# Kernel tuning notes

Hardware: AMD Instinct MI355X
Metric: run time of the kernel (lower is better)

## Reference

```python
import jax, jax.numpy as jnp
import numpy as np
from jax import lax

LN_EPS = 1e-5
DENOM_EPS = 1e-6


def taylor_exp(x, f):
    # x: [..., f] -> [..., 1 + f + f*f]
    r2 = np.sqrt(2.0).astype(np.float32)
    rd = np.sqrt(float(f)).astype(np.float32)
    rrd = np.sqrt(np.sqrt(float(f))).astype(np.float32)
    x2 = (x[..., :, None] * x[..., None, :]).reshape(*x.shape[:-1], f * f) / r2
    return jnp.concatenate([jnp.ones_like(x[..., :1]), x / rrd, x2 / rd], axis=-1)


def layer_norm(x, gamma, beta):
    mu = jnp.mean(x, axis=-1, keepdims=True)
    var = jnp.mean(jnp.square(x - mu), axis=-1, keepdims=True)
    return (x - mu) * lax.rsqrt(var + LN_EPS) * gamma + beta


def setup_inputs() -> dict:
    key = jax.random.key(0)
    ks = jax.random.split(key, 24)
    B, L, d, h, f, hd, w = 4, 2048, 1024, 16, 16, 64, 64
    D = 1 + f + f * f  # 273

    def lin_w(k, fi, fo):
        return (jax.random.normal(k, (fi, fo), jnp.float32) / np.sqrt(fi)).astype(jnp.float32)

    def lin_b(k, fo):
        return 0.01 * jax.random.normal(k, (fo,), jnp.float32)

    inp = {
        'x': jax.random.normal(ks[0], (B, L, d), jnp.float32),
        'kv_state': jnp.zeros((B, h, D, hd), jnp.float32),
        'k_state': jnp.zeros((B, h, D), jnp.float32),
        'k_buf': jnp.zeros((1, h, w, hd), jnp.float32),
        'v_buf': jnp.zeros((1, h, w, hd), jnp.float32),
        # LinearAttention projections
        'Wq_lin': lin_w(ks[1], d, f * h), 'bq_lin': lin_b(ks[2], f * h),
        'Wk_lin': lin_w(ks[3], d, f * h), 'bk_lin': lin_b(ks[4], f * h),
        'Wv_lin': lin_w(ks[5], d, hd * h), 'bv_lin': lin_b(ks[6], hd * h),
        'Wo_lin': lin_w(ks[7], d, d), 'bo_lin': lin_b(ks[8], d),
        # BasedBlock window-attention projections
        'Wq': lin_w(ks[9], d, d), 'bq': lin_b(ks[10], d),
        'Wk': lin_w(ks[11], d, d), 'bk': lin_b(ks[12], d),
        'Wv': lin_w(ks[13], d, d), 'bv': lin_b(ks[14], d),
        'Wo': lin_w(ks[15], d, d), 'bo': lin_b(ks[16], d),
        # shared LayerNorm
        'gamma': jnp.ones((d,), jnp.float32),
        'beta': jnp.zeros((d,), jnp.float32),
    }
    return inp


def reference(x, kv_state, k_state, k_buf, v_buf,
              Wq_lin, bq_lin, Wk_lin, bk_lin, Wv_lin, bv_lin, Wo_lin, bo_lin,
              Wq, bq, Wk, bk, Wv, bv, Wo, bo, gamma, beta):
    B, L, d = x.shape
    h = kv_state.shape[1]
    hd = kv_state.shape[3]
    f = Wq_lin.shape[1] // h

    # ---- LinearAttention ----
    q = (x @ Wq_lin + bq_lin).reshape(B, L, h, f).transpose(0, 2, 1, 3)   # b h l f
    k = (x @ Wk_lin + bk_lin).reshape(B, L, h, f).transpose(0, 2, 1, 3)
    v = (x @ Wv_lin + bv_lin).reshape(B, L, h, hd).transpose(0, 2, 1, 3)  # b h l hd
    qf = taylor_exp(q, f)  # b h l D
    kf = taylor_exp(k, f)

    # time-major for scan: [l, b, h, ...]
    qt = qf.transpose(2, 0, 1, 3)
    kt = kf.transpose(2, 0, 1, 3)
    vt = v.transpose(2, 0, 1, 3)

    def step(carry, inp):
        kv, kst = carry
        q_t, k_t, v_t = inp
        kv = kv + k_t[..., :, None] * v_t[..., None, :]            # b h D hd
        kst = kst + k_t                                            # b h D
        num = jnp.einsum('bhd,bhdc->bhc', q_t, kv)
        den = jnp.einsum('bhd,bhd->bh', q_t, kst) + DENOM_EPS
        return (kv, kst), num / den[..., None]

    (kv_new, k_new), outs = lax.scan(step, (kv_state, k_state), (qt, kt, vt))
    lin = outs.transpose(1, 0, 2, 3).reshape(B, L, h * hd)  # b l (h hd)
    lin_out = lin @ Wo_lin + bo_lin  # dropout is identity in eval

    x1 = layer_norm(x + lin_out, gamma, beta)

    # ---- window attention ----
    q2 = (x1 @ Wq + bq).reshape(B, L, h, hd).transpose(0, 2, 1, 3)  # b h l hd
    k2 = (x1 @ Wk + bk).reshape(B, L, h, hd).transpose(0, 2, 1, 3)
    v2 = (x1 @ Wv + bv).reshape(B, L, h, hd).transpose(0, 2, 1, 3)

    new_k = k2[:, :, -1:, :]
    new_v = v2[:, :, -1:, :]
    kb = jnp.broadcast_to(k_buf, (B,) + k_buf.shape[1:])
    vb = jnp.broadcast_to(v_buf, (B,) + v_buf.shape[1:])
    uk = jnp.concatenate([kb[:, :, 1:], new_k], axis=2)  # b h w hd
    uv = jnp.concatenate([vb[:, :, 1:], new_v], axis=2)

    scores = jnp.einsum('bhqd,bhwd->bhqw', q2, uk) / np.sqrt(float(hd))
    attn = jax.nn.softmax(scores, axis=-1)
    win = jnp.einsum('bhqw,bhwd->bhqd', attn, uv)
    win = win.transpose(0, 2, 1, 3).reshape(B, L, h * hd)

    out = layer_norm(x1 + (win @ Wo + bo), gamma, beta)
    return out, kv_new, k_new
```

## Files before the change

### kernel.cpp

```cpp
#include <hip/hip_runtime.h>
#include <math.h>


#define LL 2048
#define DD 1024
#define DFEAT 273
#define NC 16
#define CHUNK 128

typedef __attribute__((ext_vector_type(8))) short short8;
typedef __attribute__((ext_vector_type(4))) float f32x4;

#define SQ 0.42044820762685725f
#define LF 1.18920711500272107f

__device__ __forceinline__ float4 f4(float a, float b, float c, float d) {
  float4 r; r.x = a; r.y = b; r.z = c; r.w = d; return r;
}

__device__ __forceinline__ unsigned short f2bf(float f) {
  union { float f; unsigned u; } v; v.f = f;
  unsigned r = v.u + 0x7fffu + ((v.u >> 16) & 1u);
  return (unsigned short)(r >> 16);
}

__device__ __forceinline__ float bf2f(unsigned short u) {
  union { unsigned u; float f; } v; v.u = ((unsigned)u) << 16; return v.f;
}

__global__ __launch_bounds__(256) void cast_bf16(
    const float* __restrict__ in, unsigned short* __restrict__ o, int n4) {
  int i = blockIdx.x * 256 + threadIdx.x;
  if (i < n4) {
    float4 v = ((const float4*)in)[i];
    ushort4 r;
    r.x = f2bf(v.x); r.y = f2bf(v.y); r.z = f2bf(v.z); r.w = f2bf(v.w);
    ((ushort4*)o)[i] = r;
  }
}

__global__ __launch_bounds__(256) void castT(
    const float* __restrict__ W, unsigned short* __restrict__ Wt, int K, int N) {
  __shared__ float t[64][65];
  int k0 = blockIdx.x * 64, n0 = blockIdx.y * 64;
  int tid = threadIdx.x;
#pragma unroll
  for (int p = 0; p < 16; p++) {
    int idx = p * 256 + tid;
    int r = idx >> 6, c = idx & 63;
    t[r][c] = W[(size_t)(k0 + r) * N + n0 + c];
  }
  __syncthreads();
#pragma unroll
  for (int p = 0; p < 16; p++) {
    int idx = p * 256 + tid;
    int rn = idx >> 6, ck = idx & 63;
    Wt[(size_t)(n0 + rn) * K + k0 + ck] = f2bf(t[ck][rn]);
  }
}

__global__ __launch_bounds__(256) void gemm_mfma(
    const unsigned short* __restrict__ A, const unsigned short* __restrict__ Bt,
    const float* __restrict__ bias, float* __restrict__ C,
    unsigned short* __restrict__ Cb, int M, int N, int K) {
  __shared__ unsigned short As[128 * 64];
  __shared__ unsigned short Bs[128 * 64];
  const int tid = threadIdx.x;
  const int lane = tid & 63, w = tid >> 6;
  const int row0 = blockIdx.x * 128, col0 = blockIdx.y * 128;
  const int wm0 = (w & 1) * 64, wn0 = (w >> 1) * 64;
  const int lr = lane >> 3;
  const int gc = (lane & 7) ^ lr;
  const unsigned short* aP = A + (size_t)(row0 + w * 32 + lr) * K + gc * 8;
  const unsigned short* bP = Bt + (size_t)(col0 + w * 32 + lr) * K + gc * 8;
  unsigned short* asW = As + w * 2048;
  unsigned short* bsW = Bs + w * 2048;
  const int m15 = lane & 15, quad = lane >> 4;
  f32x4 acc[4][4] = {};
  for (int k0 = 0; k0 < K; k0 += 64) {
#pragma unroll
    for (int i = 0; i < 4; i++) {
      __builtin_amdgcn_global_load_lds(
          (const __attribute__((address_space(1))) unsigned int*)(const void*)(aP + (size_t)(i * 8) * K + k0),
          (__attribute__((address_space(3))) unsigned int*)(void*)(asW + i * 512), 16, 0, 0);
      __builtin_amdgcn_global_load_lds(
          (const __attribute__((address_space(1))) unsigned int*)(const void*)(bP + (size_t)(i * 8) * K + k0),
          (__attribute__((address_space(3))) unsigned int*)(void*)(bsW + i * 512), 16, 0, 0);
    }
    __syncthreads();
#pragma unroll
    for (int ks = 0; ks < 2; ks++) {
      short8 aF[4], bF[4];
#pragma unroll
      for (int mi = 0; mi < 4; mi++) {
        int r = wm0 + mi * 16 + m15;
        int g = (ks * 4 + quad) ^ (r & 7);
        aF[mi] = *(const short8*)(As + r * 64 + g * 8);
      }
#pragma unroll
      for (int ni = 0; ni < 4; ni++) {
        int r = wn0 + ni * 16 + m15;
        int g = (ks * 4 + quad) ^ (r & 7);
        bF[ni] = *(const short8*)(Bs + r * 64 + g * 8);
      }
#pragma unroll
      for (int mi = 0; mi < 4; mi++)
#pragma unroll
        for (int ni = 0; ni < 4; ni++)
          acc[mi][ni] = __builtin_amdgcn_mfma_f32_16x16x32_bf16(
              aF[mi], bF[ni], acc[mi][ni], 0, 0, 0);
    }
    __syncthreads();
  }
#pragma unroll
  for (int mi = 0; mi < 4; mi++)
#pragma unroll
    for (int ni = 0; ni < 4; ni++) {
      int col = col0 + wn0 + ni * 16 + m15;
      float bb = bias[col];
#pragma unroll
      for (int r = 0; r < 4; r++) {
        int row = row0 + wm0 + mi * 16 + quad * 4 + r;
        float val = acc[mi][ni][r] + bb;
        if (Cb) Cb[(size_t)row * N + col] = f2bf(val);
        else C[(size_t)row * N + col] = val;
      }
    }
}

__global__ __launch_bounds__(256) void transV(
    const unsigned short* __restrict__ v_b, unsigned short* __restrict__ vT) {
  __shared__ unsigned short Tv[64][72];
  const int blk = blockIdx.x;
  const int bh = blk >> 5, tt = blk & 31;
  const int b = bh >> 4, hh = bh & 15;
  const int t0 = tt * 64;
  const int tid = threadIdx.x;
  {
    int t = tid >> 2, cs = tid & 3;
    const unsigned short* p = v_b + ((size_t)(b * LL + t0 + t)) * DD + hh * 64 + cs * 16;
    *(short8*)&Tv[t][cs * 16] = *(const short8*)p;
    *(short8*)&Tv[t][cs * 16 + 8] = *(const short8*)(p + 8);
  }
  __syncthreads();
  {
    int c = tid & 63, ts = tid >> 6;
    unsigned short vals[16];
#pragma unroll
    for (int j = 0; j < 16; j++) vals[j] = Tv[ts * 16 + j][c];
    unsigned short* op = vT + ((size_t)bh * 64 + c) * LL + t0 + ts * 16;
    *(short8*)op = *(short8*)&vals[0];
    *(short8*)(op + 8) = *(short8*)&vals[8];
  }
}

__global__ __launch_bounds__(256) void phaseA2(
    const unsigned short* __restrict__ klin, const unsigned short* __restrict__ vT,
    unsigned short* __restrict__ KVc_t, unsigned short* __restrict__ kstc) {
  __shared__ unsigned short kT[16][136];
  const int tid = threadIdx.x, lane = tid & 63, w = tid >> 6;
  const int m15 = lane & 15, quad = lane >> 4;
  const int bh = blockIdx.x >> 4, ck = blockIdx.x & 15;
  const int b = bh >> 4, hh = bh & 15;
  const int t0 = ck * CHUNK;
  {
    int r = tid >> 1, half = tid & 1;
    short8 kv = *(const short8*)(klin + ((size_t)(b * LL + t0 + r)) * 256 + hh * 16 + half * 8);
#pragma unroll
    for (int j = 0; j < 8; j++)
      kT[half * 8 + j][r] = f2bf(bf2f(((unsigned short*)&kv)[j]) * SQ);
  }
  __syncthreads();
  short8 ones8 = {16256, 16256, 16256, 16256, 16256, 16256, 16256, 16256};
  short8 zer8 = {0, 0, 0, 0, 0, 0, 0, 0};
  f32x4 acc[5][5] = {};
  const unsigned short* vbase = vT + (size_t)bh * 64 * LL + t0;
#pragma unroll
  for (int ks = 0; ks < 4; ++ks) {
    const int tt = ks * 32 + quad * 8;
    short8 aF[5], bF[5];
#pragma unroll
    for (int mi = 0; mi < 5; mi++) {
      int r = (w * 5 + mi) * 16 + m15;
      short8 av;
      unsigned short* pv = (unsigned short*)&av;
      if (r == 0) {
        av = ones8;
      } else if (r < 17) {
        short8 k1 = *(const short8*)&kT[r - 1][tt];
#pragma unroll
        for (int j = 0; j < 8; j++) pv[j] = f2bf(bf2f(((unsigned short*)&k1)[j]) * LF);
      } else if (r < DFEAT) {
        int ij = r - 17;
        short8 k1 = *(const short8*)&kT[ij >> 4][tt];
        short8 k2 = *(const short8*)&kT[ij & 15][tt];
#pragma unroll
        for (int j = 0; j < 8; j++)
          pv[j] = f2bf(bf2f(((unsigned short*)&k1)[j]) * bf2f(((unsigned short*)&k2)[j]));
      } else {
        av = zer8;
      }
      aF[mi] = av;
    }
#pragma unroll
    for (int ni = 0; ni < 4; ni++)
      bF[ni] = *(const short8*)(vbase + ((size_t)(ni * 16 + m15)) * LL + tt);
    bF[4] = (m15 == 0) ? ones8 : zer8;
#pragma unroll
    for (int mi = 0; mi < 5; mi++)
#pragma unroll
      for (int ni = 0; ni < 5; ni++)
        acc[mi][ni] = __builtin_amdgcn_mfma_f32_16x16x32_bf16(
            aF[mi], bF[ni], acc[mi][ni], 0, 0, 0);
  }
  const size_t cb = ((size_t)bh * NC + ck) * (64 * 288);
  const size_t kb = ((size_t)bh * NC + ck) * 288;
#pragma unroll
  for (int mi = 0; mi < 5; mi++) {
    int fb = (w * 5 + mi) * 16 + quad * 4;
    if (fb < 288) {
#pragma unroll
      for (int ni = 0; ni < 4; ni++) {
        int c = ni * 16 + m15;
        ushort4 sv;
        sv.x = f2bf(acc[mi][ni][0]); sv.y = f2bf(acc[mi][ni][1]);
        sv.z = f2bf(acc[mi][ni][2]); sv.w = f2bf(acc[mi][ni][3]);
        *(ushort4*)(KVc_t + cb + (size_t)c * 288 + fb) = sv;
      }
      if (m15 == 0) {
        ushort4 sv;
        sv.x = f2bf(acc[mi][4][0]); sv.y = f2bf(acc[mi][4][1]);
        sv.z = f2bf(acc[mi][4][2]); sv.w = f2bf(acc[mi][4][3]);
        *(ushort4*)(kstc + kb + fb) = sv;
      }
    }
  }
}

__global__ __launch_bounds__(256) void phaseB3(
    const unsigned short* __restrict__ KVc_t, const unsigned short* __restrict__ kstc,
    const float* __restrict__ kv0, const float* __restrict__ kst0,
    unsigned short* __restrict__ KVp_t, unsigned short* __restrict__ kstp,
    float* __restrict__ kv_out, float* __restrict__ kst_out) {
  const int tid = threadIdx.x;
  if (blockIdx.x < 576) {
    int gid = blockIdx.x * 256 + tid;
    int bh = gid / 2304, rem = gid - bh * 2304;
    int c = rem / 36, fg = rem - c * 36;
    int f0 = fg * 8;
    float acc[8];
#pragma unroll
    for (int j = 0; j < 8; j++) {
      int f = f0 + j;
      acc[j] = (f < DFEAT) ? kv0[((size_t)bh * DFEAT + f) * 64 + c] : 0.0f;
    }
    size_t base = ((size_t)bh * NC) * (64 * 288) + (size_t)c * 288 + f0;
    for (int ck = 0; ck < NC; ck++) {
      size_t idx = base + (size_t)ck * (64 * 288);
      short8 t = *(const short8*)(KVc_t + idx);
      unsigned short ov[8];
#pragma unroll
      for (int j = 0; j < 8; j++) {
        ov[j] = f2bf(acc[j]);
        acc[j] += bf2f(((unsigned short*)&t)[j]);
      }
      *(short8*)(KVp_t + idx) = *(short8*)ov;
    }
#pragma unroll
    for (int j = 0; j < 8; j++) {
      int f = f0 + j;
      if (f < DFEAT) kv_out[((size_t)bh * DFEAT + f) * 64 + c] = acc[j];
    }
  } else {
    int idx0 = (blockIdx.x - 576) * 256 + tid;
    int bh = idx0 / 36, fg = idx0 - bh * 36;
    int f0 = fg * 8;
    float acc[8];
#pragma unroll
    for (int j = 0; j < 8; j++) {
      int f = f0 + j;
      acc[j] = (f < DFEAT) ? kst0[bh * DFEAT + f] : 0.0f;
    }
    for (int ck = 0; ck < NC; ck++) {
      size_t idx = ((size_t)bh * NC + ck) * 288 + f0;
      short8 t = *(const short8*)(kstc + idx);
      unsigned short ov[8];
#pragma unroll
      for (int j = 0; j < 8; j++) {
        ov[j] = f2bf(acc[j]);
        acc[j] += bf2f(((unsigned short*)&t)[j]);
      }
      *(short8*)(kstp + idx) = *(short8*)ov;
    }
#pragma unroll
    for (int j = 0; j < 8; j++) {
      int f = f0 + j;
      if (f < DFEAT) kst_out[bh * DFEAT + f] = acc[j];
    }
  }
}

__global__ __launch_bounds__(256) void phaseC4(
    const unsigned short* __restrict__ qlin, const unsigned short* __restrict__ klin,
    const unsigned short* __restrict__ vT, const unsigned short* __restrict__ KVp_t,
    const unsigned short* __restrict__ kstp, unsigned short* __restrict__ outs) {
  __shared__ float qs[4][32][36];
  __shared__ unsigned short S_l[4][32 * 128];
  const int tid = threadIdx.x, lane = tid & 63, w = tid >> 6;
  const int m15 = lane & 15, quad = lane >> 4;
  const int bh = blockIdx.x >> 4, ck = blockIdx.x & 15;
  const int qw = w;
  const int b = bh >> 4, hh = bh & 15;
  const int t0 = ck * CHUNK;
  const int tr0 = qw * 32;
  float (*qsw)[36] = qs[w];
  unsigned short* Sw = S_l[w];
  const unsigned short* qbase = qlin + ((size_t)(b * LL + t0 + tr0)) * 256 + hh * 16;
  const unsigned short* kbase = klin + ((size_t)(b * LL + t0)) * 256 + hh * 16;
  {
    int r = lane >> 1, h8 = lane & 1;
    short8 qv = *(const short8*)(qbase + (size_t)r * 256 + h8 * 8);
    float qf[8];
#pragma unroll
    for (int j = 0; j < 8; j++) qf[j] = bf2f(((unsigned short*)&qv)[j]) * SQ;
    *(float4*)&qsw[r][h8 * 8] = f4(qf[0], qf[1], qf[2], qf[3]);
    *(float4*)&qsw[r][h8 * 8 + 4] = f4(qf[4], qf[5], qf[6], qf[7]);
#pragma unroll
    for (int j = 0; j < 8; j++)
      qsw[r][16 + ((h8 * 8 + j + 9) & 15)] = qf[j];
  }
  short8 ones8 = {16256, 16256, 16256, 16256, 16256, 16256, 16256, 16256};
  short8 zer8 = {0, 0, 0, 0, 0, 0, 0, 0};
  f32x4 acc[2][5] = {};
  const unsigned short* KVb = KVp_t + ((size_t)(bh * NC + ck)) * (64 * 288);
  const unsigned short* kstb = kstp + ((size_t)(bh * NC + ck)) * 288;
#pragma unroll
  for (int ks = 0; ks < 9; ++ks) {
    const int fs = ks * 32 + quad * 8;
    short8 aF[2], bF[5];
#pragma unroll
    for (int ni = 0; ni < 4; ni++)
      bF[ni] = *(const short8*)(KVb + ((size_t)(ni * 16 + m15)) * 288 + fs);
    bF[4] = (m15 == 0) ? *(const short8*)(kstb + fs) : zer8;
#pragma unroll
    for (int mi = 0; mi < 2; mi++) {
      const float* qr = &qsw[mi * 16 + m15][0];
      unsigned short pv[8];
      if (ks == 0) {
        float qr0 = qr[0];
#pragma unroll
        for (int j = 0; j < 8; j++) {
          int f = (quad << 3) + j;
          int fl = f - 1; fl = fl < 0 ? 0 : fl;
          int fm = f - 17; fm = fm < 0 ? 0 : fm;
          float lin = qr[fl] * LF;
          float prod = qr0 * qr[fm];
          float val = (f == 0) ? 1.0f : ((f < 17) ? lin : prod);
          pv[j] = f2bf(val);
        }
      } else {
        int base = fs - 17;
        int i0 = base >> 4;
        float qi0 = qr[i0];
        float qi1 = qr[i0 + 1];
        const float* qv = qr + 16 + (base & 8);
        float qj[8];
        *(float4*)&qj[0] = *(const float4*)qv;
        *(float4*)&qj[4] = *(const float4*)(qv + 4);
        float qiB = (quad & 1) ? qi0 : qi1;
#pragma unroll
        for (int j = 0; j < 8; j++) {
          float qi = (j == 0) ? qi0 : qiB;
          float val = qi * qj[j];
          if (ks == 8) val = ((quad << 3) + j < 17) ? val : 0.0f;
          pv[j] = f2bf(val);
        }
      }
      aF[mi] = *(short8*)pv;
    }
#pragma unroll
    for (int mi = 0; mi < 2; mi++)
#pragma unroll
      for (int ni = 0; ni < 5; ni++)
        acc[mi][ni] = __builtin_amdgcn_mfma_f32_16x16x32_bf16(
            aF[mi], bF[ni], acc[mi][ni], 0, 0, 0);
  }
  const int nsn = 2 * qw + 2;
  {
    short8 aU[2], bU[8];
    aU[0] = (quad < 2) ? *(const short8*)(qbase + (size_t)m15 * 256 + quad * 8) : zer8;
    aU[1] = (quad < 2) ? *(const short8*)(qbase + (size_t)(16 + m15) * 256 + quad * 8) : zer8;
#pragma unroll
    for (int sn = 0; sn < 8; sn++) {
      if (sn < nsn) {
        int s = sn * 16 + m15;
        bU[sn] = (quad < 2) ? *(const short8*)(kbase + (size_t)s * 256 + quad * 8) : zer8;
      }
    }
#pragma unroll
    for (int mi = 0; mi < 2; mi++) {
#pragma unroll
      for (int sn = 0; sn < 8; sn++) {
        if (sn < nsn) {
          f32x4 zz = {0.f, 0.f, 0.f, 0.f};
          f32x4 u = __builtin_amdgcn_mfma_f32_16x16x32_bf16(aU[mi], bU[sn], zz, 0, 0, 0);
          int s = sn * 16 + m15;
          int gRow = s >> 3;
#pragma unroll
          for (int rr = 0; rr < 4; rr++) {
            int tl = mi * 16 + quad * 4 + rr;
            int tc = tr0 + tl;
            float uu = u[rr];
            float sv = (s <= tc) ? fmaf(uu, fmaf(uu, 0.03125f, 0.25f), 1.0f) : 0.0f;
            int p = gRow ^ (tl & 7);
            Sw[tl * 128 + p * 8 + (s & 7)] = f2bf(sv);
          }
        }
      }
    }
  }
  const unsigned short* vbase = vT + (size_t)bh * 64 * LL + t0;
#pragma unroll
  for (int ks = 0; ks < 4; ++ks) {
    if (ks <= qw) {
      const int tt = ks * 32 + quad * 8;
      short8 aF[2], bF[5];
#pragma unroll
      for (int mi = 0; mi < 2; mi++) {
        int tl = mi * 16 + m15;
        int p = (ks * 4 + quad) ^ (tl & 7);
        aF[mi] = *(const short8*)&Sw[tl * 128 + p * 8];
      }
#pragma unroll
      for (int ni = 0; ni < 4; ni++)
        bF[ni] = *(const short8*)(vbase + ((size_t)(ni * 16 + m15)) * LL + tt);
      bF[4] = (m15 == 0) ? ones8 : zer8;
#pragma unroll
      for (int mi = 0; mi < 2; mi++)
#pragma unroll
        for (int ni = 0; ni < 5; ni++)
          acc[mi][ni] = __builtin_amdgcn_mfma_f32_16x16x32_bf16(
              aF[mi], bF[ni], acc[mi][ni], 0, 0, 0);
    }
  }
#pragma unroll
  for (int mi = 0; mi < 2; mi++) {
#pragma unroll
    for (int rr = 0; rr < 4; rr++) {
      float den = __shfl(acc[mi][4][rr], (lane & 48));
      float inv = 1.0f / (den + 1e-6f);
      int tl = mi * 16 + quad * 4 + rr;
      unsigned short* op = outs + ((size_t)(b * LL + t0 + tr0 + tl)) * DD + hh * 64;
#pragma unroll
      for (int ni = 0; ni < 4; ni++)
        op[ni * 16 + m15] = f2bf(acc[mi][ni][rr] * inv);
    }
  }
}

__global__ __launch_bounds__(256) void lastrow_init(
    const float* __restrict__ bk, const float* __restrict__ bv,
    float* __restrict__ klast, float* __restrict__ vlast) {
  int gid = blockIdx.x * 256 + threadIdx.x;
  int which = gid >> 12;
  int b = (gid >> 10) & 3;
  int n = gid & 1023;
  (which ? vlast : klast)[b * 1024 + n] = which ? bv[n] : bk[n];
}

__global__ __launch_bounds__(256) void lastrow_qkv2(
    const float* __restrict__ x1,
    const float* __restrict__ Wk, const float* __restrict__ Wv,
    float* __restrict__ klast, float* __restrict__ vlast) {
  __shared__ float xs[4][64];
  __shared__ float red[4][4][64];
  const int blk = blockIdx.x;
  const int which = blk >> 8;
  const int nstrip = (blk >> 4) & 15;
  const int kslice = blk & 15;
  const int n0 = nstrip * 64, k0 = kslice * 64;
  const int tid = threadIdx.x;
  const int nn = tid & 63, p = tid >> 6;
  {
    int b = tid >> 6, k = tid & 63;
    xs[b][k] = x1[((size_t)(b * LL + LL - 1)) * DD + k0 + k];
  }
  __syncthreads();
  const float* W = which ? Wv : Wk;
  float acc[4] = {};
#pragma unroll
  for (int i = 0; i < 16; i++) {
    int kk = p * 16 + i;
    float wv = W[(size_t)(k0 + kk) * 1024 + n0 + nn];
#pragma unroll
    for (int b = 0; b < 4; b++) acc[b] = fmaf(xs[b][kk], wv, acc[b]);
  }
#pragma unroll
  for (int b = 0; b < 4; b++) red[p][b][nn] = acc[b];
  __syncthreads();
  if (p == 0) {
    float* outp = which ? vlast : klast;
#pragma unroll
    for (int b = 0; b < 4; b++) {
      float s = red[0][b][nn] + red[1][b][nn] + red[2][b][nn] + red[3][b][nn];
      atomicAdd(outp + b * 1024 + n0 + nn, s);
    }
  }
}

__global__ __launch_bounds__(256) void prep_window(
    const float* __restrict__ kbuf, const float* __restrict__ vbufw,
    const float* __restrict__ klast, const float* __restrict__ vlast,
    unsigned short* __restrict__ ukb, unsigned short* __restrict__ uvT) {
  __shared__ float Tv[64][68];
  const int bh = blockIdx.x;
  const int b = bh >> 4, hh = bh & 15;
  const int tid = threadIdx.x;
  const int wi = tid >> 2, d0 = (tid & 3) * 16;
  {
    const float* kp = (wi < 63) ? (kbuf + ((size_t)hh * 64 + wi + 1) * 64 + d0)
                                : (klast + (size_t)b * 1024 + hh * 64 + d0);
    unsigned short* op = ukb + ((size_t)bh * 64 + wi) * 64 + d0;
#pragma unroll
    for (int j4 = 0; j4 < 4; j4++) {
      float4 v = *(const float4*)(kp + j4 * 4);
      ushort4 r;
      r.x = f2bf(v.x); r.y = f2bf(v.y); r.z = f2bf(v.z); r.w = f2bf(v.w);
      *(ushort4*)(op + j4 * 4) = r;
    }
  }
  {
    const float* vp = (wi < 63) ? (vbufw + ((size_t)hh * 64 + wi + 1) * 64 + d0)
                                : (vlast + (size_t)b * 1024 + hh * 64 + d0);
#pragma unroll
    for (int j4 = 0; j4 < 4; j4++)
      *(float4*)&Tv[wi][d0 + j4 * 4] = *(const float4*)(vp + j4 * 4);
  }
  __syncthreads();
  {
    int c = tid & 63, w0 = (tid >> 6) * 16;
    unsigned short* op = uvT + ((size_t)bh * 64 + c) * 64 + w0;
    unsigned short vals[16];
#pragma unroll
    for (int j = 0; j < 16; j++) vals[j] = f2bf(Tv[w0 + j][c]);
    *(short8*)op = *(short8*)&vals[0];
    *(short8*)(op + 8) = *(short8*)&vals[8];
  }
}

__global__ __launch_bounds__(256) void window_attn2(
    const unsigned short* __restrict__ q2b, const unsigned short* __restrict__ ukb,
    const unsigned short* __restrict__ uvT, unsigned short* __restrict__ win) {
  __shared__ unsigned short S_l[128 * 64];
  const int tid = threadIdx.x, lane = tid & 63, w = tid >> 6;
  const int m15 = lane & 15, quad = lane >> 4;
  const int bh = blockIdx.x >> 4, tile = blockIdx.x & 15;
  const int b = bh >> 4, hh = bh & 15;
  const int t0 = tile * 128 + w * 32;
  const unsigned short* ukbase = ukb + (size_t)bh * 64 * 64;
  const unsigned short* uvbase = uvT + (size_t)bh * 64 * 64;
  f32x4 accS[2][4] = {};
#pragma unroll
  for (int ks = 0; ks < 2; ks++) {
    short8 aF[2], bF[4];
#pragma unroll
    for (int mi = 0; mi < 2; mi++)
      aF[mi] = *(const short8*)(q2b + ((size_t)(b * LL + t0 + mi * 16 + m15)) * DD +
                                hh * 64 + ks * 32 + quad * 8);
#pragma unroll
    for (int ni = 0; ni < 4; ni++)
      bF[ni] = *(const short8*)(ukbase + ((size_t)(ni * 16 + m15)) * 64 + ks * 32 + quad * 8);
#pragma unroll
    for (int mi = 0; mi < 2; mi++)
#pragma unroll
      for (int ni = 0; ni < 4; ni++)
        accS[mi][ni] = __builtin_amdgcn_mfma_f32_16x16x32_bf16(
            aF[mi], bF[ni], accS[mi][ni], 0, 0, 0);
  }
#pragma unroll
  for (int mi = 0; mi < 2; mi++) {
#pragma unroll
    for (int rr = 0; rr < 4; rr++) {
      float s0 = accS[mi][0][rr] * 0.125f;
      float s1 = accS[mi][1][rr] * 0.125f;
      float s2 = accS[mi][2][rr] * 0.125f;
      float s3 = accS[mi][3][rr] * 0.125f;
      float m = fmaxf(fmaxf(s0, s1), fmaxf(s2, s3));
      m = fmaxf(m, __shfl_xor(m, 1));
      m = fmaxf(m, __shfl_xor(m, 2));
      m = fmaxf(m, __shfl_xor(m, 4));
      m = fmaxf(m, __shfl_xor(m, 8));
      float p0 = __expf(s0 - m), p1 = __expf(s1 - m);
      float p2 = __expf(s2 - m), p3 = __expf(s3 - m);
      float l = p0 + p1 + p2 + p3;
      l += __shfl_xor(l, 1);
      l += __shfl_xor(l, 2);
      l += __shfl_xor(l, 4);
      l += __shfl_xor(l, 8);
      float inv = 1.0f / l;
      int tl = w * 32 + mi * 16 + quad * 4 + rr;
      int t7 = tl & 7;
      float pr[4] = {p0 * inv, p1 * inv, p2 * inv, p3 * inv};
#pragma unroll
      for (int ni = 0; ni < 4; ni++) {
        int s = ni * 16 + m15;
        S_l[tl * 64 + ((s >> 3) ^ t7) * 8 + (s & 7)] = f2bf(pr[ni]);
      }
    }
  }
  f32x4 accO[2][4] = {};
#pragma unroll
  for (int ks = 0; ks < 2; ks++) {
    short8 aF[2], bF[4];
#pragma unroll
    for (int mi = 0; mi < 2; mi++) {
      int tl = w * 32 + mi * 16 + m15;
      int g = (ks * 4 + quad) ^ (tl & 7);
      aF[mi] = *(const short8*)&S_l[tl * 64 + g * 8];
    }
#pragma unroll
    for (int ni = 0; ni < 4; ni++)
      bF[ni] = *(const short8*)(uvbase + ((size_t)(ni * 16 + m15)) * 64 + ks * 32 + quad * 8);
#pragma unroll
    for (int mi = 0; mi < 2; mi++)
#pragma unroll
      for (int ni = 0; ni < 4; ni++)
        accO[mi][ni] = __builtin_amdgcn_mfma_f32_16x16x32_bf16(
            aF[mi], bF[ni], accO[mi][ni], 0, 0, 0);
  }
#pragma unroll
  for (int mi = 0; mi < 2; mi++) {
#pragma unroll
    for (int rr = 0; rr < 4; rr++) {
      int row = t0 + mi * 16 + quad * 4 + rr;
      unsigned short* op = win + ((size_t)(b * LL + row)) * DD + hh * 64;
#pragma unroll
      for (int ni = 0; ni < 4; ni++)
        op[ni * 16 + m15] = f2bf(accO[mi][ni][rr]);
    }
  }
}

__global__ __launch_bounds__(256) void ln_add(
    const float* __restrict__ A, const float* __restrict__ Bm,
    const float* __restrict__ gamma, const float* __restrict__ beta,
    float* __restrict__ out, unsigned short* __restrict__ outb) {
  const int row = blockIdx.x, tid = threadIdx.x;
  float4 va = ((const float4*)(A + (size_t)row * DD))[tid];
  float4 vb = ((const float4*)(Bm + (size_t)row * DD))[tid];
  float4 s4 = f4(va.x + vb.x, va.y + vb.y, va.z + vb.z, va.w + vb.w);
  float s = s4.x + s4.y + s4.z + s4.w;
  float ss = s4.x * s4.x + s4.y * s4.y + s4.z * s4.z + s4.w * s4.w;
  for (int o = 32; o; o >>= 1) { s += __shfl_xor(s, o); ss += __shfl_xor(ss, o); }
  __shared__ float red[8];
  int wid = tid >> 6;
  if ((tid & 63) == 0) { red[wid * 2] = s; red[wid * 2 + 1] = ss; }
  __syncthreads();
  float tot = red[0] + red[2] + red[4] + red[6];
  float tots = red[1] + red[3] + red[5] + red[7];
  float mu = tot * (1.0f / 1024.0f);
  float var = tots * (1.0f / 1024.0f) - mu * mu;
  float rstd = rsqrtf(var + 1e-5f);
  float4 g = ((const float4*)gamma)[tid];
  float4 be = ((const float4*)beta)[tid];
  float4 o = f4((s4.x - mu) * rstd * g.x + be.x, (s4.y - mu) * rstd * g.y + be.y,
                (s4.z - mu) * rstd * g.z + be.z, (s4.w - mu) * rstd * g.w + be.w);
  ((float4*)(out + (size_t)row * DD))[tid] = o;
  if (outb) {
    ushort4 r;
    r.x = f2bf(o.x); r.y = f2bf(o.y); r.z = f2bf(o.z); r.w = f2bf(o.w);
    ((ushort4*)(outb + (size_t)row * DD))[tid] = r;
  }
}

extern "C" void kernel_launch(void* const* d_in, const int* in_sizes, int n_in,
                              void* d_out, int out_size, void* d_ws, size_t ws_size,
                              hipStream_t stream) {
  (void)in_sizes; (void)n_in; (void)out_size; (void)ws_size;
  const float* x      = (const float*)d_in[0];
  const float* kv0    = (const float*)d_in[1];
  const float* kst0   = (const float*)d_in[2];
  const float* kbuf   = (const float*)d_in[3];
  const float* vbufw  = (const float*)d_in[4];
  const float* Wq_lin = (const float*)d_in[5];
  const float* bq_lin = (const float*)d_in[6];
  const float* Wk_lin = (const float*)d_in[7];
  const float* bk_lin = (const float*)d_in[8];
  const float* Wv_lin = (const float*)d_in[9];
  const float* bv_lin = (const float*)d_in[10];
  const float* Wo_lin = (const float*)d_in[11];
  const float* bo_lin = (const float*)d_in[12];
  const float* Wq     = (const float*)d_in[13];
  const float* bq     = (const float*)d_in[14];
  const float* Wk     = (const float*)d_in[15];
  const float* bk     = (const float*)d_in[16];
  const float* Wv     = (const float*)d_in[17];
  const float* bv     = (const float*)d_in[18];
  const float* Wo     = (const float*)d_in[19];
  const float* bo     = (const float*)d_in[20];
  const float* gamma  = (const float*)d_in[21];
  const float* beta   = (const float*)d_in[22];

  float* out = (float*)d_out;
  float* kv_out  = out + 8388608;
  float* kst_out = out + 8388608 + 1118208;

  float* ws = (float*)d_ws;
  const size_t MF = 1024 * 1024;
  unsigned short* qlin_b = (unsigned short*)(ws);
  unsigned short* klin_b = (unsigned short*)(ws + 1 * MF);
  unsigned short* v_b    = (unsigned short*)(ws + 2 * MF);
  unsigned short* vT     = (unsigned short*)(ws + 6 * MF);
  unsigned short* KVc_t  = (unsigned short*)(ws + 10 * MF);
  unsigned short* kstc   = (unsigned short*)(ws + 19 * MF);
  unsigned short* KVp_t  = (unsigned short*)(ws + 20 * MF);
  unsigned short* kstp   = (unsigned short*)(ws + 29 * MF);
  unsigned short* x_bf   = (unsigned short*)(ws + 30 * MF);
  unsigned short* outs_bf = (unsigned short*)(ws + 2 * MF);
  float* tmp  = ws + 10 * MF;
  float* x1   = ws + 20 * MF;
  unsigned short* x1b = (unsigned short*)(ws + 30 * MF);
  unsigned short* q2b = (unsigned short*)ws;
  unsigned short* winb = (unsigned short*)(ws + 8 * MF);
  float* tmp2 = ws + 12 * MF;
  float* klast = ws + 34 * MF;
  float* vlast = klast + 4096;
  unsigned short* ukb = (unsigned short*)(ws + 34 * MF + 8192);
  unsigned short* uvTw = ukb + 262144;
  unsigned short* WtQL = (unsigned short*)(ws + 35 * MF);
  unsigned short* WtKL = WtQL + 262144;
  unsigned short* WtVL = WtQL + 524288;
  unsigned short* WtO1 = WtQL + 1572864;
  unsigned short* WtQ2 = WtQL + 2621440;
  unsigned short* WtO2 = WtQL + 3670016;

  dim3 blk(256);
  cast_bf16<<<8192, blk, 0, stream>>>(x, x_bf, 2097152);
  castT<<<dim3(16, 4), blk, 0, stream>>>(Wq_lin, WtQL, 1024, 256);
  castT<<<dim3(16, 4), blk, 0, stream>>>(Wk_lin, WtKL, 1024, 256);
  castT<<<dim3(16, 16), blk, 0, stream>>>(Wv_lin, WtVL, 1024, 1024);
  castT<<<dim3(16, 16), blk, 0, stream>>>(Wo_lin, WtO1, 1024, 1024);
  castT<<<dim3(16, 16), blk, 0, stream>>>(Wq, WtQ2, 1024, 1024);
  castT<<<dim3(16, 16), blk, 0, stream>>>(Wo, WtO2, 1024, 1024);
  gemm_mfma<<<dim3(64, 2), blk, 0, stream>>>(x_bf, WtQL, bq_lin, (float*)0, qlin_b, 8192, 256, 1024);
  gemm_mfma<<<dim3(64, 2), blk, 0, stream>>>(x_bf, WtKL, bk_lin, (float*)0, klin_b, 8192, 256, 1024);
  gemm_mfma<<<dim3(64, 8), blk, 0, stream>>>(x_bf, WtVL, bv_lin, (float*)0, v_b, 8192, 1024, 1024);
  transV<<<2048, blk, 0, stream>>>(v_b, vT);
  phaseA2<<<1024, blk, 0, stream>>>(klin_b, vT, KVc_t, kstc);
  phaseB3<<<585, blk, 0, stream>>>(KVc_t, kstc, kv0, kst0, KVp_t, kstp, kv_out, kst_out);
  phaseC4<<<1024, blk, 0, stream>>>(qlin_b, klin_b, vT, KVp_t, kstp, outs_bf);
  gemm_mfma<<<dim3(64, 8), blk, 0, stream>>>(outs_bf, WtO1, bo_lin, tmp, (unsigned short*)0, 8192, 1024, 1024);
  ln_add<<<8192, blk, 0, stream>>>(x, tmp, gamma, beta, x1, x1b);
  gemm_mfma<<<dim3(64, 8), blk, 0, stream>>>(x1b, WtQ2, bq, (float*)0, q2b, 8192, 1024, 1024);
  lastrow_init<<<32, blk, 0, stream>>>(bk, bv, klast, vlast);
  lastrow_qkv2<<<512, blk, 0, stream>>>(x1, Wk, Wv, klast, vlast);
  prep_window<<<64, blk, 0, stream>>>(kbuf, vbufw, klast, vlast, ukb, uvTw);
  window_attn2<<<1024, blk, 0, stream>>>(q2b, ukb, uvTw, winb);
  gemm_mfma<<<dim3(64, 8), blk, 0, stream>>>(winb, WtO2, bo, tmp2, (unsigned short*)0, 8192, 1024, 1024);
  ln_add<<<8192, blk, 0, stream>>>(x1, tmp2, gamma, beta, out, (unsigned short*)0);
}
```

Measured before the change: 443.4 us.

## Fuse QKV projection GEMMs, batch weight casts, and use bf16 intermediates

Merges the six weight-transpose-cast launches into one kernel that also concatenates the q/k/v biases. The three linear-attention projections become a single N=1536 GEMM, and downstream kernels index into the combined output. The output-projection GEMMs and the first layernorm now write bf16 instead of fp32, and the second layernorm and last-row projection read the bf16 x1. This cuts launch count and memory traffic, at the cost of extra bf16 rounding in the residual path (x1 is now kept only in bf16).

```diff
diff --git a/kernel.cpp b/kernel.cpp
--- a/kernel.cpp
+++ b/kernel.cpp
@@ -7,6 +7,7 @@
 #define DFEAT 273
 #define NC 16
 #define CHUNK 128
+#define QKVN 1536
 
 typedef __attribute__((ext_vector_type(8))) short short8;
 typedef __attribute__((ext_vector_type(4))) float f32x4;
@@ -39,11 +40,31 @@
   }
 }
 
-__global__ __launch_bounds__(256) void castT(
-    const float* __restrict__ W, unsigned short* __restrict__ Wt, int K, int N) {
+__global__ __launch_bounds__(256) void castT_all(
+    const float* __restrict__ Wql, const float* __restrict__ Wkl,
+    const float* __restrict__ Wvl, const float* __restrict__ Wo1,
+    const float* __restrict__ Wq2, const float* __restrict__ Wo2,
+    const float* __restrict__ bql, const float* __restrict__ bkl,
+    const float* __restrict__ bvl,
+    unsigned short* __restrict__ Wcomb, unsigned short* __restrict__ WtO1,
+    unsigned short* __restrict__ WtQ2, unsigned short* __restrict__ WtO2,
+    float* __restrict__ bqkv) {
   __shared__ float t[64][65];
-  int k0 = blockIdx.x * 64, n0 = blockIdx.y * 64;
-  int tid = threadIdx.x;
+  const int blk = blockIdx.x, tid = threadIdx.x;
+  if (blk < 6) {
+    int i = blk * 256 + tid;
+    float v = (i < 256) ? bql[i] : (i < 512) ? bkl[i - 256] : bvl[i - 512];
+    bqkv[i] = v;
+  }
+  const float* W; unsigned short* Wt; int N, t0;
+  if (blk < 64)       { W = Wql; Wt = Wcomb;               N = 256;  t0 = blk; }
+  else if (blk < 128) { W = Wkl; Wt = Wcomb + 256 * 1024;  N = 256;  t0 = blk - 64; }
+  else if (blk < 384) { W = Wvl; Wt = Wcomb + 512 * 1024;  N = 1024; t0 = blk - 128; }
+  else if (blk < 640) { W = Wo1; Wt = WtO1;                N = 1024; t0 = blk - 384; }
+  else if (blk < 896) { W = Wq2; Wt = WtQ2;                N = 1024; t0 = blk - 640; }
+  else                { W = Wo2; Wt = WtO2;                N = 1024; t0 = blk - 896; }
+  const int nt = N >> 6;
+  const int k0 = (t0 / nt) * 64, n0 = (t0 % nt) * 64;
 #pragma unroll
   for (int p = 0; p < 16; p++) {
     int idx = p * 256 + tid;
@@ -55,7 +76,7 @@
   for (int p = 0; p < 16; p++) {
     int idx = p * 256 + tid;
     int rn = idx >> 6, ck = idx & 63;
-    Wt[(size_t)(n0 + rn) * K + k0 + ck] = f2bf(t[ck][rn]);
+    Wt[(size_t)(n0 + rn) * 1024 + k0 + ck] = f2bf(t[ck][rn]);
   }
 }
 
@@ -129,7 +150,7 @@
 }
 
 __global__ __launch_bounds__(256) void transV(
-    const unsigned short* __restrict__ v_b, unsigned short* __restrict__ vT) {
+    const unsigned short* __restrict__ qkv, unsigned short* __restrict__ vT) {
   __shared__ unsigned short Tv[64][72];
   const int blk = blockIdx.x;
   const int bh = blk >> 5, tt = blk & 31;
@@ -138,7 +159,7 @@
   const int tid = threadIdx.x;
   {
     int t = tid >> 2, cs = tid & 3;
-    const unsigned short* p = v_b + ((size_t)(b * LL + t0 + t)) * DD + hh * 64 + cs * 16;
+    const unsigned short* p = qkv + ((size_t)(b * LL + t0 + t)) * QKVN + 512 + hh * 64 + cs * 16;
     *(short8*)&Tv[t][cs * 16] = *(const short8*)p;
     *(short8*)&Tv[t][cs * 16 + 8] = *(const short8*)(p + 8);
   }
@@ -155,7 +176,7 @@
 }
 
 __global__ __launch_bounds__(256) void phaseA2(
-    const unsigned short* __restrict__ klin, const unsigned short* __restrict__ vT,
+    const unsigned short* __restrict__ qkv, const unsigned short* __restrict__ vT,
     unsigned short* __restrict__ KVc_t, unsigned short* __restrict__ kstc) {
   __shared__ unsigned short kT[16][136];
   const int tid = threadIdx.x, lane = tid & 63, w = tid >> 6;
@@ -165,7 +186,7 @@
   const int t0 = ck * CHUNK;
   {
     int r = tid >> 1, half = tid & 1;
-    short8 kv = *(const short8*)(klin + ((size_t)(b * LL + t0 + r)) * 256 + hh * 16 + half * 8);
+    short8 kv = *(const short8*)(qkv + ((size_t)(b * LL + t0 + r)) * QKVN + 256 + hh * 16 + half * 8);
 #pragma unroll
     for (int j = 0; j < 8; j++)
       kT[half * 8 + j][r] = f2bf(bf2f(((unsigned short*)&kv)[j]) * SQ);
@@ -301,7 +322,7 @@
 }
 
 __global__ __launch_bounds__(256) void phaseC4(
-    const unsigned short* __restrict__ qlin, const unsigned short* __restrict__ klin,
+    const unsigned short* __restrict__ qkv,
     const unsigned short* __restrict__ vT, const unsigned short* __restrict__ KVp_t,
     const unsigned short* __restrict__ kstp, unsigned short* __restrict__ outs) {
   __shared__ float qs[4][32][36];
@@ -315,11 +336,11 @@
   const int tr0 = qw * 32;
   float (*qsw)[36] = qs[w];
   unsigned short* Sw = S_l[w];
-  const unsigned short* qbase = qlin + ((size_t)(b * LL + t0 + tr0)) * 256 + hh * 16;
-  const unsigned short* kbase = klin + ((size_t)(b * LL + t0)) * 256 + hh * 16;
+  const unsigned short* qbase = qkv + ((size_t)(b * LL + t0 + tr0)) * QKVN + hh * 16;
+  const unsigned short* kbase = qkv + ((size_t)(b * LL + t0)) * QKVN + 256 + hh * 16;
   {
     int r = lane >> 1, h8 = lane & 1;
-    short8 qv = *(const short8*)(qbase + (size_t)r * 256 + h8 * 8);
+    short8 qv = *(const short8*)(qbase + (size_t)r * QKVN + h8 * 8);
     float qf[8];
 #pragma unroll
     for (int j = 0; j < 8; j++) qf[j] = bf2f(((unsigned short*)&qv)[j]) * SQ;
@@ -388,13 +409,13 @@
   const int nsn = 2 * qw + 2;
   {
     short8 aU[2], bU[8];
-    aU[0] = (quad < 2) ? *(const short8*)(qbase + (size_t)m15 * 256 + quad * 8) : zer8;
-    aU[1] = (quad < 2) ? *(const short8*)(qbase + (size_t)(16 + m15) * 256 + quad * 8) : zer8;
+    aU[0] = (quad < 2) ? *(const short8*)(qbase + (size_t)m15 * QKVN + quad * 8) : zer8;
+    aU[1] = (quad < 2) ? *(const short8*)(qbase + (size_t)(16 + m15) * QKVN + quad * 8) : zer8;
 #pragma unroll
     for (int sn = 0; sn < 8; sn++) {
       if (sn < nsn) {
         int s = sn * 16 + m15;
-        bU[sn] = (quad < 2) ? *(const short8*)(kbase + (size_t)s * 256 + quad * 8) : zer8;
+        bU[sn] = (quad < 2) ? *(const short8*)(kbase + (size_t)s * QKVN + quad * 8) : zer8;
       }
     }
 #pragma unroll
@@ -469,7 +490,7 @@
 }
 
 __global__ __launch_bounds__(256) void lastrow_qkv2(
-    const float* __restrict__ x1,
+    const unsigned short* __restrict__ x1b,
     const float* __restrict__ Wk, const float* __restrict__ Wv,
     float* __restrict__ klast, float* __restrict__ vlast) {
   __shared__ float xs[4][64];
@@ -483,7 +504,7 @@
   const int nn = tid & 63, p = tid >> 6;
   {
     int b = tid >> 6, k = tid & 63;
-    xs[b][k] = x1[((size_t)(b * LL + LL - 1)) * DD + k0 + k];
+    xs[b][k] = bf2f(x1b[((size_t)(b * LL + LL - 1)) * DD + k0 + k]);
   }
   __syncthreads();
   const float* W = which ? Wv : Wk;
@@ -641,14 +662,22 @@
   }
 }
 
-__global__ __launch_bounds__(256) void ln_add(
-    const float* __restrict__ A, const float* __restrict__ Bm,
+__global__ __launch_bounds__(256) void ln_add2(
+    const float* __restrict__ Af, const unsigned short* __restrict__ Ab,
+    const unsigned short* __restrict__ Bmb,
     const float* __restrict__ gamma, const float* __restrict__ beta,
     float* __restrict__ out, unsigned short* __restrict__ outb) {
   const int row = blockIdx.x, tid = threadIdx.x;
-  float4 va = ((const float4*)(A + (size_t)row * DD))[tid];
-  float4 vb = ((const float4*)(Bm + (size_t)row * DD))[tid];
-  float4 s4 = f4(va.x + vb.x, va.y + vb.y, va.z + vb.z, va.w + vb.w);
+  float a0, a1, a2, a3;
+  if (Af) {
+    float4 va = ((const float4*)(Af + (size_t)row * DD))[tid];
+    a0 = va.x; a1 = va.y; a2 = va.z; a3 = va.w;
+  } else {
+    ushort4 ua = ((const ushort4*)(Ab + (size_t)row * DD))[tid];
+    a0 = bf2f(ua.x); a1 = bf2f(ua.y); a2 = bf2f(ua.z); a3 = bf2f(ua.w);
+  }
+  ushort4 ub = ((const ushort4*)(Bmb + (size_t)row * DD))[tid];
+  float4 s4 = f4(a0 + bf2f(ub.x), a1 + bf2f(ub.y), a2 + bf2f(ub.z), a3 + bf2f(ub.w));
   float s = s4.x + s4.y + s4.z + s4.w;
   float ss = s4.x * s4.x + s4.y * s4.y + s4.z * s4.z + s4.w * s4.w;
   for (int o = 32; o; o >>= 1) { s += __shfl_xor(s, o); ss += __shfl_xor(ss, o); }
@@ -665,7 +694,7 @@
   float4 be = ((const float4*)beta)[tid];
   float4 o = f4((s4.x - mu) * rstd * g.x + be.x, (s4.y - mu) * rstd * g.y + be.y,
                 (s4.z - mu) * rstd * g.z + be.z, (s4.w - mu) * rstd * g.w + be.w);
-  ((float4*)(out + (size_t)row * DD))[tid] = o;
+  if (out) ((float4*)(out + (size_t)row * DD))[tid] = o;
   if (outb) {
     ushort4 r;
     r.x = f2bf(o.x); r.y = f2bf(o.y); r.z = f2bf(o.z); r.w = f2bf(o.w);
@@ -707,55 +736,46 @@
 
   float* ws = (float*)d_ws;
   const size_t MF = 1024 * 1024;
-  unsigned short* qlin_b = (unsigned short*)(ws);
-  unsigned short* klin_b = (unsigned short*)(ws + 1 * MF);
-  unsigned short* v_b    = (unsigned short*)(ws + 2 * MF);
-  unsigned short* vT     = (unsigned short*)(ws + 6 * MF);
-  unsigned short* KVc_t  = (unsigned short*)(ws + 10 * MF);
-  unsigned short* kstc   = (unsigned short*)(ws + 19 * MF);
-  unsigned short* KVp_t  = (unsigned short*)(ws + 20 * MF);
-  unsigned short* kstp   = (unsigned short*)(ws + 29 * MF);
-  unsigned short* x_bf   = (unsigned short*)(ws + 30 * MF);
-  unsigned short* outs_bf = (unsigned short*)(ws + 2 * MF);
-  float* tmp  = ws + 10 * MF;
-  float* x1   = ws + 20 * MF;
-  unsigned short* x1b = (unsigned short*)(ws + 30 * MF);
-  unsigned short* q2b = (unsigned short*)ws;
-  unsigned short* winb = (unsigned short*)(ws + 8 * MF);
-  float* tmp2 = ws + 12 * MF;
-  float* klast = ws + 34 * MF;
+  unsigned short* x_bf   = (unsigned short*)(ws);
+  unsigned short* qkv_b  = (unsigned short*)(ws + 4 * MF);
+  unsigned short* vT     = (unsigned short*)(ws + 10 * MF);
+  unsigned short* KVc_t  = (unsigned short*)(ws + 14 * MF);
+  unsigned short* kstc   = (unsigned short*)(ws + 23 * MF);
+  unsigned short* KVp_t  = (unsigned short*)(ws + 24 * MF);
+  unsigned short* kstp   = (unsigned short*)(ws + 33 * MF);
+  unsigned short* outs_bf = (unsigned short*)(ws + 34 * MF);
+  unsigned short* tmp_b  = (unsigned short*)(ws + 38 * MF);
+  unsigned short* x1b    = (unsigned short*)(ws + 42 * MF);
+  unsigned short* q2b    = (unsigned short*)(ws + 46 * MF);
+  unsigned short* winb   = (unsigned short*)(ws + 50 * MF);
+  unsigned short* tmp2_b = (unsigned short*)(ws + 54 * MF);
+  float* klast = ws + 58 * MF;
   float* vlast = klast + 4096;
-  unsigned short* ukb = (unsigned short*)(ws + 34 * MF + 8192);
+  unsigned short* ukb  = (unsigned short*)(ws + 58 * MF + 8192);
   unsigned short* uvTw = ukb + 262144;
-  unsigned short* WtQL = (unsigned short*)(ws + 35 * MF);
-  unsigned short* WtKL = WtQL + 262144;
-  unsigned short* WtVL = WtQL + 524288;
-  unsigned short* WtO1 = WtQL + 1572864;
-  unsigned short* WtQ2 = WtQL + 2621440;
-  unsigned short* WtO2 = WtQL + 3670016;
+  unsigned short* Wcomb = (unsigned short*)(ws + 59 * MF);
+  unsigned short* WtO1  = (unsigned short*)(ws + 60 * MF);
+  unsigned short* WtQ2  = (unsigned short*)(ws + 61 * MF);
+  unsigned short* WtO2  = (unsigned short*)(ws + 62 * MF);
+  float* bqkv = ws + 63 * MF;
 
   dim3 blk(256);
   cast_bf16<<<8192, blk, 0, stream>>>(x, x_bf, 2097152);
-  castT<<<dim3(16, 4), blk, 0, stream>>>(Wq_lin, WtQL, 1024, 256);
-  castT<<<dim3(16, 4), blk, 0, stream>>>(Wk_lin, WtKL, 1024, 256);
-  castT<<<dim3(16, 16), blk, 0, stream>>>(Wv_lin, WtVL, 1024, 1024);
-  castT<<<dim3(16, 16), blk, 0, stream>>>(Wo_lin, WtO1, 1024, 1024);
-  castT<<<dim3(16, 16), blk, 0, stream>>>(Wq, WtQ2, 1024, 1024);
-  castT<<<dim3(16, 16), blk, 0, stream>>>(Wo, WtO2, 1024, 1024);
-  gemm_mfma<<<dim3(64, 2), blk, 0, stream>>>(x_bf, WtQL, bq_lin, (float*)0, qlin_b, 8192, 256, 1024);
-  gemm_mfma<<<dim3(64, 2), blk, 0, stream>>>(x_bf, WtKL, bk_lin, (float*)0, klin_b, 8192, 256, 1024);
-  gemm_mfma<<<dim3(64, 8), blk, 0, stream>>>(x_bf, WtVL, bv_lin, (float*)0, v_b, 8192, 1024, 1024);
-  transV<<<2048, blk, 0, stream>>>(v_b, vT);
-  phaseA2<<<1024, blk, 0, stream>>>(klin_b, vT, KVc_t, kstc);
+  castT_all<<<1152, blk, 0, stream>>>(Wq_lin, Wk_lin, Wv_lin, Wo_lin, Wq, Wo,
+                                      bq_lin, bk_lin, bv_lin,
+                                      Wcomb, WtO1, WtQ2, WtO2, bqkv);
+  gemm_mfma<<<dim3(64, 12), blk, 0, stream>>>(x_bf, Wcomb, bqkv, (float*)0, qkv_b, 8192, QKVN, 1024);
+  transV<<<2048, blk, 0, stream>>>(qkv_b, vT);
+  phaseA2<<<1024, blk, 0, stream>>>(qkv_b, vT, KVc_t, kstc);
   phaseB3<<<585, blk, 0, stream>>>(KVc_t, kstc, kv0, kst0, KVp_t, kstp, kv_out, kst_out);
-  phaseC4<<<1024, blk, 0, stream>>>(qlin_b, klin_b, vT, KVp_t, kstp, outs_bf);
-  gemm_mfma<<<dim3(64, 8), blk, 0, stream>>>(outs_bf, WtO1, bo_lin, tmp, (unsigned short*)0, 8192, 1024, 1024);
-  ln_add<<<8192, blk, 0, stream>>>(x, tmp, gamma, beta, x1, x1b);
+  phaseC4<<<1024, blk, 0, stream>>>(qkv_b, vT, KVp_t, kstp, outs_bf);
+  gemm_mfma<<<dim3(64, 8), blk, 0, stream>>>(outs_bf, WtO1, bo_lin, (float*)0, tmp_b, 8192, 1024, 1024);
+  ln_add2<<<8192, blk, 0, stream>>>(x, (const unsigned short*)0, tmp_b, gamma, beta, (float*)0, x1b);
   gemm_mfma<<<dim3(64, 8), blk, 0, stream>>>(x1b, WtQ2, bq, (float*)0, q2b, 8192, 1024, 1024);
   lastrow_init<<<32, blk, 0, stream>>>(bk, bv, klast, vlast);
-  lastrow_qkv2<<<512, blk, 0, stream>>>(x1, Wk, Wv, klast, vlast);
+  lastrow_qkv2<<<512, blk, 0, stream>>>(x1b, Wk, Wv, klast, vlast);
   prep_window<<<64, blk, 0, stream>>>(kbuf, vbufw, klast, vlast, ukb, uvTw);
   window_attn2<<<1024, blk, 0, stream>>>(q2b, ukb, uvTw, winb);
-  gemm_mfma<<<dim3(64, 8), blk, 0, stream>>>(winb, WtO2, bo, tmp2, (unsigned short*)0, 8192, 1024, 1024);
-  ln_add<<<8192, blk, 0, stream>>>(x1, tmp2, gamma, beta, out, (unsigned short*)0);
-}
+  gemm_mfma<<<dim3(64, 8), blk, 0, stream>>>(winb, WtO2, bo, (float*)0, tmp2_b, 8192, 1024, 1024);
+  ln_add2<<<8192, blk, 0, stream>>>((const float*)0, x1b, tmp2_b, gamma, beta, out, (unsigned short*)0);
+}
```

After: 388.9 us. 1.14x faster.
